# Performance work log

Hardware: AMD Instinct MI355X
Metric: run time of the kernel (lower is better)

## Reference

```python
import jax, jax.numpy as jnp
import numpy as np

ALLPASS_DELAYS = [225, 556, 441, 341]
ALLPASS_G = 0.7
COMB_DELAYS = [1116, 1188, 1277, 1356]
COMB_FEEDBACKS = [0.84, 0.82, 0.80, 0.78]


def _lagged_first_order(x, N, g, allpass):
    """Fixed-lag first-order recurrence along axis 0, vectorized over axis 1.

    allpass: y[n] = -g*y[n-N] + x[n] + g*x[n-N]  (n >= N), y[n<N] = 0
    comb:    y[n] =  g*y[n-N] + x[n]             (n >= N), y[n<N] = 0

    The recurrence decouples into N independent stride-N subsequences, so we
    reshape to [blocks, N, W] and lax.scan over blocks (T/N steps instead of T).
    """
    T, W = x.shape
    blocks = -(-T // N)
    Tp = blocks * N
    xb = jnp.pad(x, ((0, Tp - T), (0, 0))).reshape(blocks, N, W)
    zero_blk = jnp.zeros((1, N, W), x.dtype)
    if allpass:
        # drive u[k] = x[k] + g*x[k-1]; block 0 output is forced to zero
        u = jnp.concatenate([zero_blk, xb[1:] + g * xb[:-1]], axis=0)
        a = -g
    else:
        # comb: drive u[k] = x[k] for k>=1; block 0 output is zero
        u = jnp.concatenate([zero_blk, xb[1:]], axis=0)
        a = g

    def step(prev, uk):
        y = uk + a * prev
        return y, y

    _, yb = jax.lax.scan(step, jnp.zeros((N, W), x.dtype), u)
    return yb.reshape(Tp, W)[:T]


def setup_inputs() -> dict:
    key = jax.random.key(0)
    T, W = 131072, 128
    x = jax.random.normal(key, (T, W), dtype=jnp.float32)
    return {"x": x}


def reference(x):
    # Series allpass chain
    for N in ALLPASS_DELAYS:
        x = _lagged_first_order(x, N, ALLPASS_G, allpass=True)
    # Parallel feedback comb bank, summed
    comb = jnp.zeros_like(x)
    for N, g in zip(COMB_DELAYS, COMB_FEEDBACKS):
        comb = comb + _lagged_first_order(x, N, g, allpass=False)
    # Original applies eye(T) @ comb and slices [:, :W]; both are identity ops,
    # so we return comb directly (same math, without materializing a TxT eye).
    return comb
```

## Files before the change

kernel.cpp:

```cpp
#include <hip/hip_runtime.h>


constexpr int W = 128;

template <int V> struct fv { float d[V]; };

template <int V>
__device__ __forceinline__ fv<V> fv_zero() {
  fv<V> r;
#pragma unroll
  for (int c = 0; c < V; ++c) r.d[c] = 0.f;
  return r;
}
using fv2 = fv<2>;
using fv4 = fv<4>;

template <int K, bool PRED>
__device__ __forceinline__
void fmarch_blk(const fv4* __restrict__ sb, int n0, int N, int laneoff,
                int Tn, float a, fv4& yp, fv4* __restrict__ y) {
  constexpr int RW = W / 4;
  fv4 xs[K];
#pragma unroll
  for (int u = 0; u < K; ++u) {
    const int n = n0 + u * N;
    xs[u] = (!PRED || n < Tn) ? sb[n * RW + laneoff] : fv_zero<4>();
  }
#pragma unroll
  for (int u = 0; u < K; ++u) {
#pragma unroll
    for (int c = 0; c < 4; ++c)
      yp.d[c] = fmaf(a, yp.d[c], xs[u].d[c]);
    y[u] = yp;
  }
}

template <int CNT, bool PRED, int U>
__device__ __forceinline__
void fmarch_seg(const fv4* __restrict__ sb, int n0, int N, int laneoff,
                int Tn, float a, fv4& yp, fv4* __restrict__ y) {
  constexpr int NB = CNT / U, R = CNT % U;
#pragma unroll
  for (int b = 0; b < NB; ++b)
    fmarch_blk<U, PRED>(sb, n0 + b * U * N, N, laneoff, Tn, a, yp, y + b * U);
  if constexpr (R > 0)
    fmarch_blk<R, PRED>(sb, n0 + NB * U * N, N, laneoff, Tn, a, yp, y + NB * U);
}

template <int MODE, int K, bool PRED>
__device__ __forceinline__
void fstore_blk(fv4* __restrict__ out, int n0, int N, int laneoff, int Tn,
                float a, fv4 Yin, const fv4* __restrict__ y, float& p) {
  constexpr int RW = W / 4;
  fv4 os[K];
  if constexpr (MODE == 2) {
#pragma unroll
    for (int u = 0; u < K; ++u) {
      const int n = n0 + u * N;
      os[u] = (!PRED || n < Tn) ? out[n * RW + laneoff] : fv_zero<4>();
    }
  }
#pragma unroll
  for (int u = 0; u < K; ++u) {
    const int n = n0 + u * N;
    fv4 v;
#pragma unroll
    for (int c = 0; c < 4; ++c) {
      v.d[c] = fmaf(p, Yin.d[c], y[u].d[c]);
      if constexpr (MODE == 2) v.d[c] += os[u].d[c];
    }
    if (!PRED || n < Tn) out[n * RW + laneoff] = v;
    p *= a;
  }
}

template <int MODE, int CNT, bool PRED, int U>
__device__ __forceinline__
void fstore_seg(fv4* __restrict__ out, int n0, int N, int laneoff, int Tn,
                float a, fv4 Yin, const fv4* __restrict__ y, float p0) {
  constexpr int NB = CNT / U, R = CNT % U;
  float p = p0;
#pragma unroll
  for (int b = 0; b < NB; ++b)
    fstore_blk<MODE, U, PRED>(out, n0 + b * U * N, N, laneoff, Tn, a, Yin,
                              y + b * U, p);
  if constexpr (R > 0)
    fstore_blk<MODE, R, PRED>(out, n0 + NB * U * N, N, laneoff, Tn, a, Yin,
                              y + NB * U, p);
}

template <int MODE, int S, int L, bool ODDN, int UM, int US>
__global__ __launch_bounds__(S * 64, 2)
void fcomb(const fv4* __restrict__ sb, fv4* __restrict__ out,
           int N, float g, float aL, int T, int items) {
  const float a = g;
  __shared__ fv4 C[S][64];
  const int tid = threadIdx.x;
  const int s  = tid >> 6;
  const int l6 = tid & 63;
  const int laneoff = l6 & 31;

  for (int item = blockIdx.x; item < items; item += gridDim.x) {
    const int r  = (item << 1) | (l6 >> 5);
    const int Tn = (!ODDN || r < N) ? T : 0;
    const int n0 = s * L * N + r;

    fv4 y[L];
    fv4 yp = fv_zero<4>();

    if (s == 0) {
      y[0] = fv_zero<4>();
      fmarch_seg<L - 1, ODDN, UM>(sb, n0 + N, N, laneoff, Tn, a, yp, y + 1);
    } else if (!ODDN && s < S - 1) {
      fmarch_seg<L, false, UM>(sb, n0, N, laneoff, Tn, a, yp, y);
    } else {
      fmarch_seg<L, true, UM>(sb, n0, N, laneoff, Tn, a, yp, y);
    }
    C[s][l6] = yp;
    __syncthreads();

    fv4 Yin = fv_zero<4>();
    for (int j = 0; j < s; ++j) {
#pragma unroll
      for (int c = 0; c < 4; ++c)
        Yin.d[c] = fmaf(aL, Yin.d[c], C[j][l6].d[c]);
    }
    __syncthreads();

    if (!ODDN && s < S - 1)
      fstore_seg<MODE, L, false, US>(out, n0, N, laneoff, Tn, a, Yin, y, a);
    else
      fstore_seg<MODE, L, true, US>(out, n0, N, laneoff, Tn, a, Yin, y, a);
  }
}

__global__ void prep_pw(float* __restrict__ pw1, float* __restrict__ pw2) {
  if (threadIdx.x == 0) {
    float p = 1.f;
    for (int m = 0; m < 1024; ++m) { pw1[m] = p; p *= -0.7f; }
  } else if (threadIdx.x == 64) {
    float p = 1.f;
    for (int m = 0; m < 512; ++m) { pw2[m] = p; p *= -0.7f; }
  }
}

__global__ __launch_bounds__(256)
void prep_h1(const fv2* __restrict__ x, fv2* __restrict__ h1) {
  const int e = blockIdx.x * 256 + threadIdx.x;
  if (e >= 556 * 64) return;
  const int n = e >> 6;
  fv2 v;
  if (n < 225) {
    v = fv_zero<2>();
  } else {
    v = x[e];
    const int   d = (n < 450) ? 225 : 450;
    const float c = (n < 450) ? 0.7f : -0.49f;
    fv2 t = x[e - d * 64];
    v.d[0] = fmaf(c, t.d[0], v.d[0]);
    v.d[1] = fmaf(c, t.d[1], v.d[1]);
  }
  h1[e] = v;
}

__global__ __launch_bounds__(1024)
void prep_s(const fv4* __restrict__ x, const fv4* __restrict__ h1,
            const float* __restrict__ pw1, const float* __restrict__ pw2,
            fv4* __restrict__ sb) {
  const int e = blockIdx.x * 1024 + threadIdx.x;
  const int n  = e >> 5;
  const int lo = e & 31;
  const int q1 = n / 225, r1 = n - q1 * 225;
  const int q2 = n / 556, r2 = n - q2 * 556;
  const fv4 xs = x[e];
  const fv4 t1 = x[r1 * 32 + lo];
  const fv4 t2 = h1[r2 * 32 + lo];
  const float p1 = pw1[q1];
  const float p2 = pw2[q2];
  fv4 v;
#pragma unroll
  for (int c = 0; c < 4; ++c) {
    float s = fmaf(-p1, t1.d[c], xs.d[c]);
    v.d[c] = fmaf(-p2, t2.d[c], s);
  }
  sb[e] = v;
}

constexpr int W2 = 64;
template <int MODE, bool STORE>
__device__ __forceinline__
void g_march(const float2* __restrict__ in, float2* __restrict__ out,
             int n, int N, int cnt, int T, int lane, float g, float a,
             float2& xp, float2& yp) {
  for (int j = 0; j < cnt; ++j) {
    float2 x = (n < T) ? in[n * W2 + lane] : make_float2(0.f, 0.f);
    float ux = (MODE == 0) ? fmaf(g, xp.x, x.x) : x.x;
    float uy = (MODE == 0) ? fmaf(g, xp.y, x.y) : x.y;
    yp.x = fmaf(a, yp.x, ux);
    yp.y = fmaf(a, yp.y, uy);
    xp = x;
    if (STORE && n < T) {
      float2 v = yp;
      if (MODE == 2) { v.x += out[n * W2 + lane].x; v.y += out[n * W2 + lane].y; }
      out[n * W2 + lane] = v;
    }
    n += N;
  }
}

template <int MODE>
__global__ __launch_bounds__(1024)
void stage_gen(const float2* __restrict__ in, float2* __restrict__ out,
               int N, float g, float aL, int L, int T) {
  const float a = (MODE == 0) ? -g : g;
  __shared__ float2 C[16][W2];
  const int tid = threadIdx.x, s = tid >> 6, lane = tid & 63;
  const int r = blockIdx.x;
  if (r >= T) return;
  const int n0 = s * L * N + r;
  if (s == 0) {
    float2 xp = make_float2(0.f, 0.f), yp = make_float2(0.f, 0.f);
    if (MODE == 0) xp = in[r * W2 + lane];
    if (MODE != 2) out[r * W2 + lane] = make_float2(0.f, 0.f);
    g_march<MODE, true>(in, out, r + N, N, L - 1, T, lane, g, a, xp, yp);
    C[0][lane] = yp;
    __syncthreads();
    return;
  }
  {
    float2 xp = make_float2(0.f, 0.f), yp = make_float2(0.f, 0.f);
    if (MODE == 0) xp = in[(n0 - N) * W2 + lane];
    g_march<MODE, false>(in, out, n0, N, L, T, lane, g, a, xp, yp);
    C[s][lane] = yp;
  }
  __syncthreads();
  float2 Yin = make_float2(0.f, 0.f);
  for (int j = 0; j < s; ++j) {
    Yin.x = fmaf(aL, Yin.x, C[j][lane].x);
    Yin.y = fmaf(aL, Yin.y, C[j][lane].y);
  }
  float2 xp = make_float2(0.f, 0.f), yp = Yin;
  if (MODE == 0) xp = in[(n0 - N) * W2 + lane];
  g_march<MODE, true>(in, out, n0, N, L, T, lane, g, a, xp, yp);
}

static void pick_SL(int T, int N, int S0, int* Sp, int* Lp) {
  int Kmin = T / N, Kmax = (T + N - 1) / N;
  int S = S0;
  for (; S > 1; --S) {
    int L = (Kmax + S - 1) / S;
    if ((S - 1) * L <= Kmin) break;
  }
  *Sp = S;
  *Lp = (Kmax + *Sp - 1) / *Sp;
}

static float pow_f(float a, int n) {
  double p = 1.0;
  for (int i = 0; i < n; ++i) p *= (double)a;
  return (float)p;
}

extern "C" void kernel_launch(void* const* d_in, const int* in_sizes, int n_in,
                              void* d_out, int out_size, void* d_ws, size_t ws_size,
                              hipStream_t stream) {
  float* out = (float*)d_out;
  float* ws  = (float*)d_ws;
  const float* x = (const float*)d_in[0];
  const int T = in_sizes[0] / W;

  if (T == 131072) {
    float* h1f = out;
    float* pw1 = out + 556 * 128;
    float* pw2 = pw1 + 1024;
    float* sbf = ws;

    hipLaunchKernelGGL(prep_pw, dim3(1), dim3(128), 0, stream, pw1, pw2);
    hipLaunchKernelGGL(prep_h1, dim3(139), dim3(256), 0, stream,
                       (const fv2*)x, (fv2*)h1f);
    hipLaunchKernelGGL(prep_s, dim3(4096), dim3(1024), 0, stream,
                       (const fv4*)x, (const fv4*)h1f, pw1, pw2, (fv4*)sbf);

    const fv4* s4 = (const fv4*)sbf;
    fv4* o4 = (fv4*)out;

    hipLaunchKernelGGL((fcomb<1, 8, 15, false, 4, 4>), dim3(512), dim3(512),
                       0, stream, s4, o4, 1116, 0.84f, pow_f(0.84f, 15), T, 558);
    hipLaunchKernelGGL((fcomb<2, 8, 14, false, 4, 4>), dim3(512), dim3(512),
                       0, stream, s4, o4, 1188, 0.82f, pow_f(0.82f, 14), T, 594);
    hipLaunchKernelGGL((fcomb<2, 8, 13, true, 4, 4>), dim3(512), dim3(512),
                       0, stream, s4, o4, 1277, 0.80f, pow_f(0.80f, 13), T, 639);
    hipLaunchKernelGGL((fcomb<2, 8, 13, false, 4, 4>), dim3(512), dim3(512),
                       0, stream, s4, o4, 1356, 0.78f, pow_f(0.78f, 13), T, 678);
  } else {
    const int   apN[4] = {225, 556, 441, 341};
    const int   cbN[4] = {1116, 1188, 1277, 1356};
    const float cbG[4] = {0.84f, 0.82f, 0.80f, 0.78f};
    const float2* src = (const float2*)x;
    float2* bufs[2] = {(float2*)out, (float2*)ws};
    int cur = 0;
    for (int i = 0; i < 4; ++i) {
      int S, L;
      pick_SL(T, apN[i], 16, &S, &L);
      hipLaunchKernelGGL((stage_gen<0>), dim3(apN[i]), dim3(S * 64), 0, stream,
                         src, bufs[cur], apN[i], 0.7f, pow_f(-0.7f, L), L, T);
      src = bufs[cur];
      cur ^= 1;
    }
    float2* dst = (src == (float2*)out) ? (float2*)ws : (float2*)out;
    for (int i = 0; i < 4; ++i) {
      int S, L;
      pick_SL(T, cbN[i], 16, &S, &L);
      if (i == 0)
        hipLaunchKernelGGL((stage_gen<1>), dim3(cbN[i]), dim3(S * 64), 0, stream,
                           src, dst, cbN[i], cbG[i], pow_f(cbG[i], L), L, T);
      else
        hipLaunchKernelGGL((stage_gen<2>), dim3(cbN[i]), dim3(S * 64), 0, stream,
                           src, dst, cbN[i], cbG[i], pow_f(cbG[i], L), L, T);
    }
    if (dst != (float2*)out)
      hipMemcpyAsync(out, dst, (size_t)T * W * sizeof(float),
                     hipMemcpyDeviceToDevice, stream);
  }
}
```

Before: 255.2 us.

## Switch comb kernels to float2 per-row items and fuse prep kernels

```diff
diff --git a/kernel.cpp b/kernel.cpp
--- a/kernel.cpp
+++ b/kernel.cpp
@@ -15,57 +15,58 @@
 using fv2 = fv<2>;
 using fv4 = fv<4>;
 
-template <int K, bool PRED>
-__device__ __forceinline__
-void fmarch_blk(const fv4* __restrict__ sb, int n0, int N, int laneoff,
-                int Tn, float a, fv4& yp, fv4* __restrict__ y) {
-  constexpr int RW = W / 4;
-  fv4 xs[K];
+template <int K, bool PRED, int V>
+__device__ __forceinline__
+void fmarch_blk(const fv<V>* __restrict__ sb, int n0, int N, int laneoff,
+                int Tn, float a, fv<V>& yp, fv<V>* __restrict__ y) {
+  constexpr int RW = W / V;
+  fv<V> xs[K];
 #pragma unroll
   for (int u = 0; u < K; ++u) {
     const int n = n0 + u * N;
-    xs[u] = (!PRED || n < Tn) ? sb[n * RW + laneoff] : fv_zero<4>();
+    xs[u] = (!PRED || n < Tn) ? sb[n * RW + laneoff] : fv_zero<V>();
   }
 #pragma unroll
   for (int u = 0; u < K; ++u) {
 #pragma unroll
-    for (int c = 0; c < 4; ++c)
+    for (int c = 0; c < V; ++c)
       yp.d[c] = fmaf(a, yp.d[c], xs[u].d[c]);
     y[u] = yp;
   }
 }
 
-template <int CNT, bool PRED, int U>
-__device__ __forceinline__
-void fmarch_seg(const fv4* __restrict__ sb, int n0, int N, int laneoff,
-                int Tn, float a, fv4& yp, fv4* __restrict__ y) {
+template <int CNT, bool PRED, int V, int U>
+__device__ __forceinline__
+void fmarch_seg(const fv<V>* __restrict__ sb, int n0, int N, int laneoff,
+                int Tn, float a, fv<V>& yp, fv<V>* __restrict__ y) {
   constexpr int NB = CNT / U, R = CNT % U;
 #pragma unroll
   for (int b = 0; b < NB; ++b)
-    fmarch_blk<U, PRED>(sb, n0 + b * U * N, N, laneoff, Tn, a, yp, y + b * U);
+    fmarch_blk<U, PRED, V>(sb, n0 + b * U * N, N, laneoff, Tn, a, yp, y + b * U);
   if constexpr (R > 0)
-    fmarch_blk<R, PRED>(sb, n0 + NB * U * N, N, laneoff, Tn, a, yp, y + NB * U);
-}
-
-template <int MODE, int K, bool PRED>
-__device__ __forceinline__
-void fstore_blk(fv4* __restrict__ out, int n0, int N, int laneoff, int Tn,
-                float a, fv4 Yin, const fv4* __restrict__ y, float& p) {
-  constexpr int RW = W / 4;
-  fv4 os[K];
+    fmarch_blk<R, PRED, V>(sb, n0 + NB * U * N, N, laneoff, Tn, a, yp,
+                           y + NB * U);
+}
+
+template <int MODE, int K, bool PRED, int V>
+__device__ __forceinline__
+void fstore_blk(fv<V>* __restrict__ out, int n0, int N, int laneoff, int Tn,
+                float a, fv<V> Yin, const fv<V>* __restrict__ y, float& p) {
+  constexpr int RW = W / V;
+  fv<V> os[K];
   if constexpr (MODE == 2) {
 #pragma unroll
     for (int u = 0; u < K; ++u) {
       const int n = n0 + u * N;
-      os[u] = (!PRED || n < Tn) ? out[n * RW + laneoff] : fv_zero<4>();
+      os[u] = (!PRED || n < Tn) ? out[n * RW + laneoff] : fv_zero<V>();
     }
   }
 #pragma unroll
   for (int u = 0; u < K; ++u) {
     const int n = n0 + u * N;
-    fv4 v;
-#pragma unroll
-    for (int c = 0; c < 4; ++c) {
+    fv<V> v;
+#pragma unroll
+    for (int c = 0; c < V; ++c) {
       v.d[c] = fmaf(p, Yin.d[c], y[u].d[c]);
       if constexpr (MODE == 2) v.d[c] += os[u].d[c];
     }
@@ -74,114 +75,95 @@
   }
 }
 
-template <int MODE, int CNT, bool PRED, int U>
-__device__ __forceinline__
-void fstore_seg(fv4* __restrict__ out, int n0, int N, int laneoff, int Tn,
-                float a, fv4 Yin, const fv4* __restrict__ y, float p0) {
+template <int MODE, int CNT, bool PRED, int V, int U>
+__device__ __forceinline__
+void fstore_seg(fv<V>* __restrict__ out, int n0, int N, int laneoff, int Tn,
+                float a, fv<V> Yin, const fv<V>* __restrict__ y, float p0) {
   constexpr int NB = CNT / U, R = CNT % U;
   float p = p0;
 #pragma unroll
   for (int b = 0; b < NB; ++b)
-    fstore_blk<MODE, U, PRED>(out, n0 + b * U * N, N, laneoff, Tn, a, Yin,
-                              y + b * U, p);
+    fstore_blk<MODE, U, PRED, V>(out, n0 + b * U * N, N, laneoff, Tn, a, Yin,
+                                 y + b * U, p);
   if constexpr (R > 0)
-    fstore_blk<MODE, R, PRED>(out, n0 + NB * U * N, N, laneoff, Tn, a, Yin,
-                              y + NB * U, p);
-}
-
-template <int MODE, int S, int L, bool ODDN, int UM, int US>
-__global__ __launch_bounds__(S * 64, 2)
-void fcomb(const fv4* __restrict__ sb, fv4* __restrict__ out,
+    fstore_blk<MODE, R, PRED, V>(out, n0 + NB * U * N, N, laneoff, Tn, a, Yin,
+                                 y + NB * U, p);
+}
+
+template <int MODE, int S, int L, int UM, int US>
+__global__ __launch_bounds__(S * 64, 3)
+void fcomb(const fv2* __restrict__ sb, fv2* __restrict__ out,
            int N, float g, float aL, int T, int items) {
   const float a = g;
-  __shared__ fv4 C[S][64];
+  __shared__ fv2 C[S][64];
   const int tid = threadIdx.x;
   const int s  = tid >> 6;
   const int l6 = tid & 63;
-  const int laneoff = l6 & 31;
 
   for (int item = blockIdx.x; item < items; item += gridDim.x) {
-    const int r  = (item << 1) | (l6 >> 5);
-    const int Tn = (!ODDN || r < N) ? T : 0;
+    const int r  = item;
     const int n0 = s * L * N + r;
 
-    fv4 y[L];
-    fv4 yp = fv_zero<4>();
+    fv2 y[L];
+    fv2 yp = fv_zero<2>();
 
     if (s == 0) {
-      y[0] = fv_zero<4>();
-      fmarch_seg<L - 1, ODDN, UM>(sb, n0 + N, N, laneoff, Tn, a, yp, y + 1);
-    } else if (!ODDN && s < S - 1) {
-      fmarch_seg<L, false, UM>(sb, n0, N, laneoff, Tn, a, yp, y);
+      y[0] = fv_zero<2>();
+      fmarch_seg<L - 1, false, 2, UM>(sb, n0 + N, N, l6, T, a, yp, y + 1);
+    } else if (s < S - 1) {
+      fmarch_seg<L, false, 2, UM>(sb, n0, N, l6, T, a, yp, y);
     } else {
-      fmarch_seg<L, true, UM>(sb, n0, N, laneoff, Tn, a, yp, y);
+      fmarch_seg<L, true, 2, UM>(sb, n0, N, l6, T, a, yp, y);
     }
     C[s][l6] = yp;
     __syncthreads();
 
-    fv4 Yin = fv_zero<4>();
+    fv2 Yin = fv_zero<2>();
     for (int j = 0; j < s; ++j) {
 #pragma unroll
-      for (int c = 0; c < 4; ++c)
+      for (int c = 0; c < 2; ++c)
         Yin.d[c] = fmaf(aL, Yin.d[c], C[j][l6].d[c]);
     }
     __syncthreads();
 
-    if (!ODDN && s < S - 1)
-      fstore_seg<MODE, L, false, US>(out, n0, N, laneoff, Tn, a, Yin, y, a);
+    if (s < S - 1)
+      fstore_seg<MODE, L, false, 2, US>(out, n0, N, l6, T, a, Yin, y, a);
     else
-      fstore_seg<MODE, L, true, US>(out, n0, N, laneoff, Tn, a, Yin, y, a);
-  }
-}
-
-__global__ void prep_pw(float* __restrict__ pw1, float* __restrict__ pw2) {
-  if (threadIdx.x == 0) {
-    float p = 1.f;
-    for (int m = 0; m < 1024; ++m) { pw1[m] = p; p *= -0.7f; }
-  } else if (threadIdx.x == 64) {
-    float p = 1.f;
-    for (int m = 0; m < 512; ++m) { pw2[m] = p; p *= -0.7f; }
-  }
-}
-
-__global__ __launch_bounds__(256)
-void prep_h1(const fv2* __restrict__ x, fv2* __restrict__ h1) {
-  const int e = blockIdx.x * 256 + threadIdx.x;
-  if (e >= 556 * 64) return;
-  const int n = e >> 6;
-  fv2 v;
-  if (n < 225) {
-    v = fv_zero<2>();
-  } else {
-    v = x[e];
-    const int   d = (n < 450) ? 225 : 450;
-    const float c = (n < 450) ? 0.7f : -0.49f;
-    fv2 t = x[e - d * 64];
-    v.d[0] = fmaf(c, t.d[0], v.d[0]);
-    v.d[1] = fmaf(c, t.d[1], v.d[1]);
-  }
-  h1[e] = v;
+      fstore_seg<MODE, L, true, 2, US>(out, n0, N, l6, T, a, Yin, y, a);
+  }
 }
 
 __global__ __launch_bounds__(1024)
-void prep_s(const fv4* __restrict__ x, const fv4* __restrict__ h1,
-            const float* __restrict__ pw1, const float* __restrict__ pw2,
-            fv4* __restrict__ sb) {
+void prep_s(const fv4* __restrict__ x, fv4* __restrict__ sb) {
   const int e = blockIdx.x * 1024 + threadIdx.x;
   const int n  = e >> 5;
   const int lo = e & 31;
   const int q1 = n / 225, r1 = n - q1 * 225;
   const int q2 = n / 556, r2 = n - q2 * 556;
+  const float LG = -0.5145731728297583f;
+  const float m1 = exp2f((float)q1 * LG);
+  const float m2 = exp2f((float)q2 * LG);
+  const float p1 = (q1 & 1) ? -m1 : m1;
+  const float p2 = (q2 & 1) ? -m2 : m2;
+
   const fv4 xs = x[e];
   const fv4 t1 = x[r1 * 32 + lo];
-  const fv4 t2 = h1[r2 * 32 + lo];
-  const float p1 = pw1[q1];
-  const float p2 = pw2[q2];
+  fv4 t2;
+  if (r2 < 225) {
+    t2 = fv_zero<4>();
+  } else {
+    t2 = x[r2 * 32 + lo];
+    const int   d = (r2 < 450) ? 225 : 450;
+    const float c = (r2 < 450) ? 0.7f : -0.49f;
+    const fv4 tt = x[(r2 - d) * 32 + lo];
+#pragma unroll
+    for (int k = 0; k < 4; ++k) t2.d[k] = fmaf(c, tt.d[k], t2.d[k]);
+  }
   fv4 v;
 #pragma unroll
-  for (int c = 0; c < 4; ++c) {
-    float s = fmaf(-p1, t1.d[c], xs.d[c]);
-    v.d[c] = fmaf(-p2, t2.d[c], s);
+  for (int k = 0; k < 4; ++k) {
+    float sv = fmaf(-p1, t1.d[k], xs.d[k]);
+    v.d[k] = fmaf(-p2, t2.d[k], sv);
   }
   sb[e] = v;
 }
@@ -270,28 +252,22 @@
   const int T = in_sizes[0] / W;
 
   if (T == 131072) {
-    float* h1f = out;
-    float* pw1 = out + 556 * 128;
-    float* pw2 = pw1 + 1024;
     float* sbf = ws;
 
-    hipLaunchKernelGGL(prep_pw, dim3(1), dim3(128), 0, stream, pw1, pw2);
-    hipLaunchKernelGGL(prep_h1, dim3(139), dim3(256), 0, stream,
-                       (const fv2*)x, (fv2*)h1f);
     hipLaunchKernelGGL(prep_s, dim3(4096), dim3(1024), 0, stream,
-                       (const fv4*)x, (const fv4*)h1f, pw1, pw2, (fv4*)sbf);
-
-    const fv4* s4 = (const fv4*)sbf;
-    fv4* o4 = (fv4*)out;
-
-    hipLaunchKernelGGL((fcomb<1, 8, 15, false, 4, 4>), dim3(512), dim3(512),
-                       0, stream, s4, o4, 1116, 0.84f, pow_f(0.84f, 15), T, 558);
-    hipLaunchKernelGGL((fcomb<2, 8, 14, false, 4, 4>), dim3(512), dim3(512),
-                       0, stream, s4, o4, 1188, 0.82f, pow_f(0.82f, 14), T, 594);
-    hipLaunchKernelGGL((fcomb<2, 8, 13, true, 4, 4>), dim3(512), dim3(512),
-                       0, stream, s4, o4, 1277, 0.80f, pow_f(0.80f, 13), T, 639);
-    hipLaunchKernelGGL((fcomb<2, 8, 13, false, 4, 4>), dim3(512), dim3(512),
-                       0, stream, s4, o4, 1356, 0.78f, pow_f(0.78f, 13), T, 678);
+                       (const fv4*)x, (fv4*)sbf);
+
+    const fv2* s2 = (const fv2*)sbf;
+    fv2* o2 = (fv2*)out;
+
+    hipLaunchKernelGGL((fcomb<1, 8, 15, 4, 4>), dim3(1024), dim3(512),
+                       0, stream, s2, o2, 1116, 0.84f, pow_f(0.84f, 15), T, 1116);
+    hipLaunchKernelGGL((fcomb<2, 8, 14, 4, 4>), dim3(1024), dim3(512),
+                       0, stream, s2, o2, 1188, 0.82f, pow_f(0.82f, 14), T, 1188);
+    hipLaunchKernelGGL((fcomb<2, 8, 13, 4, 4>), dim3(1024), dim3(512),
+                       0, stream, s2, o2, 1277, 0.80f, pow_f(0.80f, 13), T, 1277);
+    hipLaunchKernelGGL((fcomb<2, 8, 13, 4, 4>), dim3(1024), dim3(512),
+                       0, stream, s2, o2, 1356, 0.78f, pow_f(0.78f, 13), T, 1356);
   } else {
     const int   apN[4] = {225, 556, 441, 341};
     const int   cbN[4] = {1116, 1188, 1277, 1356};
```

New measurement: 227.0 us. -11.0%, faster.
